# Kernel optimization log

Hardware: AMD Instinct MI355X
Metric: run time of the kernel (lower is better)

Reference implementation:

```python
import jax, jax.numpy as jnp
import numpy as np

MARGIN = 1.9
SQUARED = False


def _pairwise_distances(e, squared):
    # e: [n, d]
    dot = e @ e.T                      # [n, n]
    sq = jnp.diagonal(dot)             # [n]
    d = jax.nn.relu(sq[None, :] - 2.0 * dot + sq[:, None])
    if not squared:
        zero_mask = (d == 0.0).astype(d.dtype)
        d = jnp.sqrt(d + zero_mask * 1e-16) * (1.0 - zero_mask)
    return d


def setup_inputs() -> dict:
    key = jax.random.key(0)
    k1, k2 = jax.random.split(key)
    embeddings = jax.random.normal(k1, (8, 80, 128), dtype=jnp.float32)
    labels = jax.random.randint(k2, (8, 80), 0, 10, dtype=jnp.int64)
    return {"embeddings": embeddings, "labels": labels}


def reference(embeddings, labels):
    b, s, dim = embeddings.shape
    e = embeddings.reshape(-1, dim)          # [n, d]
    lab = labels.reshape(-1)                 # [n]
    n = e.shape[0]

    dist = _pairwise_distances(e, SQUARED)   # [n, n]

    labels_equal = lab[None, :] == lab[:, None]
    not_diag = ~jnp.eye(n, dtype=bool)
    positive_mask = labels_equal & not_diag  # [n, n]
    negative_mask = ~labels_equal            # [n, n]

    # triplet tensor [anchor i, positive j, negative k]
    triplet = dist[:, :, None] - dist[:, None, :] + MARGIN  # [n, n, n]
    valid = positive_mask[:, :, None] & negative_mask[:, None, :]
    non_easy = valid & (triplet > 0)

    num_valid = valid.sum().astype(jnp.float32)
    num_non_easy = non_easy.sum().astype(jnp.float32)

    total = jnp.sum(triplet * non_easy.astype(triplet.dtype))
    loss = jnp.where(num_non_easy > 0, total / jnp.maximum(num_non_easy, 1.0), 0.0)
    frac = num_non_easy / (num_valid + 1e-16)
    return loss, num_valid, num_non_easy, frac
```

## Files before the change

kernel.cpp:

```cpp
#include <hip/hip_runtime.h>
#include <math.h>

#define MARGIN 1.9f
#define NMAX 1024
#define COLS 64

__global__ __launch_bounds__(256) void fused_triplet_kernel(
        const float* __restrict__ e, const int* __restrict__ lab,
        int n, int d,
        float* __restrict__ part_sum,
        unsigned int* __restrict__ part_ne,
        unsigned int* __restrict__ part_valid)
{
    __shared__ float4 Bs4[COLS * 33];
    __shared__ float  part[4 * 68];
    __shared__ float  row[NMAX];
    __shared__ float  pos[NMAX];
    __shared__ int    labs[NMAX];
    __shared__ int p_cnt, n_cnt;
    __shared__ float red_s[4];
    __shared__ unsigned int red_c[4];

    const int i    = blockIdx.x;
    const int tid  = threadIdx.x;
    const int lane = tid & 63;
    const int wv   = tid >> 6;
    const int nf4  = d >> 2;

    if (tid == 0) { p_cnt = 0; n_cnt = 0; }
    for (int j = tid; j < n; j += 256) labs[j] = lab[j];

    const float4* eg = (const float4*)e;
    float4 ai[8];
    {
        const float4* ep = eg + (size_t)i * nf4 + wv * 8;
#pragma unroll
        for (int t = 0; t < 8; ++t) ai[t] = ep[t];
    }

    const int nrounds = (n + COLS - 1) / COLS;
    for (int r = 0; r < nrounds; ++r) {
        const int col0 = r * COLS;
#pragma unroll
        for (int k = 0; k < 8; ++k) {
            int idx = tid + 256 * k;
            int rr = idx >> 5, c4 = idx & 31;
            int g = col0 + rr; if (g >= n) g = n - 1;
            Bs4[rr * 33 + c4] = eg[(size_t)g * nf4 + c4];
        }
        __syncthreads();
        const float4* bp = &Bs4[lane * 33 + wv * 8];
        float acc = 0.f;
#pragma unroll
        for (int t = 0; t < 8; ++t) {
            float4 b = bp[t];
            float4 a = ai[t];
            float dx;
            dx = a.x - b.x; acc = fmaf(dx, dx, acc);
            dx = a.y - b.y; acc = fmaf(dx, dx, acc);
            dx = a.z - b.z; acc = fmaf(dx, dx, acc);
            dx = a.w - b.w; acc = fmaf(dx, dx, acc);
        }
        part[wv * 68 + lane] = acc;
        __syncthreads();
        if (wv == 0) {
            float v = part[lane] + part[68 + lane] + part[136 + lane] + part[204 + lane];
            int c = col0 + lane;
            if (c < n) row[c] = (v == 0.f) ? 0.f : sqrtf(v);
        }
        __syncthreads();
    }

    const int my_lab = labs[i];
    int local_neg = 0;
    for (int j = tid; j < n; j += 256) {
        if (labs[j] == my_lab) {
            if (j != i) { int k = atomicAdd(&p_cnt, 1); pos[k] = row[j]; }
        } else {
            local_neg++;
        }
    }
    for (int off = 32; off > 0; off >>= 1) local_neg += __shfl_down(local_neg, off, 64);
    if (lane == 0) atomicAdd(&n_cnt, local_neg);

    const float INF = __builtin_huge_valf();
    int j0 = tid, j1 = tid + 256, j2 = tid + 512, j3 = tid + 768;
    float n0 = (j0 < n && labs[j0] != my_lab) ? row[j0] : INF;
    float n1 = (j1 < n && labs[j1] != my_lab) ? row[j1] : INF;
    float n2 = (j2 < n && labs[j2] != my_lab) ? row[j2] : INF;
    float n3 = (j3 < n && labs[j3] != my_lab) ? row[j3] : INF;
    __syncthreads();
    const int P = p_cnt, N = n_cnt;

    float sum = 0.f;
    unsigned int c = 0;
    for (int j = 0; j < P; ++j) {
        float a = pos[j] + MARGIN;
        float t0 = a - n0; if (t0 > 0.f) { sum += t0; c++; }
        float t1 = a - n1; if (t1 > 0.f) { sum += t1; c++; }
        float t2 = a - n2; if (t2 > 0.f) { sum += t2; c++; }
        float t3 = a - n3; if (t3 > 0.f) { sum += t3; c++; }
    }

    for (int off = 32; off > 0; off >>= 1) {
        sum += __shfl_down(sum, off, 64);
        c   += __shfl_down(c,   off, 64);
    }
    if (lane == 0) { red_s[wv] = sum; red_c[wv] = c; }
    __syncthreads();
    if (tid == 0) {
        float s = 0.f; unsigned int cc = 0;
        for (int w = 0; w < 4; ++w) { s += red_s[w]; cc += red_c[w]; }
        part_sum[i]   = s;
        part_ne[i]    = cc;
        part_valid[i] = (unsigned int)P * (unsigned int)N;
    }
}

__global__ __launch_bounds__(256) void finalize_kernel(
        const float* __restrict__ part_sum,
        const unsigned int* __restrict__ part_ne,
        const unsigned int* __restrict__ part_valid,
        int nblk, float* __restrict__ out)
{
    __shared__ float red_s[4];
    __shared__ unsigned long long red_ne[4], red_nv[4];
    int tid = threadIdx.x;

    float s = 0.f;
    unsigned long long ne = 0, nv = 0;
    for (int b = tid; b < nblk; b += blockDim.x) {
        s  += part_sum[b];
        ne += part_ne[b];
        nv += part_valid[b];
    }
    for (int off = 32; off > 0; off >>= 1) {
        s  += __shfl_down(s,  off, 64);
        ne += __shfl_down(ne, off, 64);
        nv += __shfl_down(nv, off, 64);
    }
    int wave = tid >> 6;
    if ((tid & 63) == 0) { red_s[wave] = s; red_ne[wave] = ne; red_nv[wave] = nv; }
    __syncthreads();
    if (tid == 0) {
        float ts = 0.f; unsigned long long tne = 0, tnv = 0;
        int nwaves = (blockDim.x + 63) >> 6;
        for (int w = 0; w < nwaves; ++w) { ts += red_s[w]; tne += red_ne[w]; tnv += red_nv[w]; }
        float fne = (float)tne;
        float fnv = (float)tnv;
        out[0] = (fne > 0.f) ? (ts / fmaxf(fne, 1.f)) : 0.f;
        out[1] = fnv;
        out[2] = fne;
        out[3] = fne / (fnv + 1e-16f);
    }
}

extern "C" void kernel_launch(void* const* d_in, const int* in_sizes, int n_in,
                              void* d_out, int out_size, void* d_ws, size_t ws_size,
                              hipStream_t stream) {
    const float* e  = (const float*)d_in[0];
    const int* lab  = (const int*)d_in[1];
    int n = in_sizes[1];
    int d = in_sizes[0] / n;

    char* ws = (char*)d_ws;
    float*        part_sum   = (float*)ws;
    unsigned int* part_ne    = (unsigned int*)(ws + (size_t)n * 4);
    unsigned int* part_valid = (unsigned int*)(ws + (size_t)n * 8);

    fused_triplet_kernel<<<n, 256, 0, stream>>>(e, lab, n, d,
                                                part_sum, part_ne, part_valid);
    finalize_kernel<<<1, 256, 0, stream>>>(part_sum, part_ne, part_valid,
                                           n, (float*)d_out);
}
```

Baseline: 76.53 us.

## Process four anchors per block, one wave per anchor, with ballot-based positive compaction

Each block now handles four anchor rows: every wave computes one anchor's full distance row over the whole feature dimension, so the cross-wave partial reduction and its extra barriers go away. Each column tile loaded into shared memory is reused by four anchors, which cuts global and LDS traffic by four. Positives are compacted per wave with ballot/popcount instead of shared atomics, and negatives are kept in registers across 10 slots. The risks are a hard cap of 640 rows and 192 positives per anchor, plus fewer blocks (160) for the GPU, and each wave now runs the triplet loop for a single anchor.

```diff
diff --git a/kernel.cpp b/kernel.cpp
--- a/kernel.cpp
+++ b/kernel.cpp
@@ -2,118 +2,124 @@
 #include <math.h>
 
 #define MARGIN 1.9f
-#define NMAX 1024
-#define COLS 64
+#define NMAX  640
+#define NSLOT 10
+#define ACH   4
+#define PCAP  192
 
-__global__ __launch_bounds__(256) void fused_triplet_kernel(
+__global__ __launch_bounds__(256) void fused_strip_kernel(
         const float* __restrict__ e, const int* __restrict__ lab,
         int n, int d,
         float* __restrict__ part_sum,
         unsigned int* __restrict__ part_ne,
         unsigned int* __restrict__ part_valid)
 {
-    __shared__ float4 Bs4[COLS * 33];
-    __shared__ float  part[4 * 68];
-    __shared__ float  row[NMAX];
-    __shared__ float  pos[NMAX];
     __shared__ int    labs[NMAX];
-    __shared__ int p_cnt, n_cnt;
-    __shared__ float red_s[4];
-    __shared__ unsigned int red_c[4];
+    __shared__ float4 As4[ACH * 32];
+    __shared__ float4 Bs4[64 * 33];
+    __shared__ float  rows[ACH][NMAX];
+    __shared__ float  pos[ACH][PCAP];
 
-    const int i    = blockIdx.x;
     const int tid  = threadIdx.x;
     const int lane = tid & 63;
     const int wv   = tid >> 6;
+    const int i0   = blockIdx.x * ACH;
     const int nf4  = d >> 2;
 
-    if (tid == 0) { p_cnt = 0; n_cnt = 0; }
     for (int j = tid; j < n; j += 256) labs[j] = lab[j];
+    const float4* eg = (const float4*)e;
+    if (tid < ACH * nf4) {
+        int a  = tid / nf4;
+        int c4 = tid - a * nf4;
+        int gi = i0 + a; if (gi >= n) gi = n - 1;
+        As4[a * 32 + c4] = eg[(size_t)gi * nf4 + c4];
+    }
+    __syncthreads();
 
-    const float4* eg = (const float4*)e;
-    float4 ai[8];
-    {
-        const float4* ep = eg + (size_t)i * nf4 + wv * 8;
-#pragma unroll
-        for (int t = 0; t < 8; ++t) ai[t] = ep[t];
-    }
-
-    const int nrounds = (n + COLS - 1) / COLS;
-    for (int r = 0; r < nrounds; ++r) {
-        const int col0 = r * COLS;
+    const int ntile = (n + 63) >> 6;
+    for (int tt = 0; tt < ntile; ++tt) {
+        const int col0 = tt << 6;
 #pragma unroll
         for (int k = 0; k < 8; ++k) {
-            int idx = tid + 256 * k;
-            int rr = idx >> 5, c4 = idx & 31;
-            int g = col0 + rr; if (g >= n) g = n - 1;
-            Bs4[rr * 33 + c4] = eg[(size_t)g * nf4 + c4];
+            int idx = tid + (k << 8);
+            int r = idx >> 5, c4 = idx & 31;
+            if (c4 < nf4) {
+                int g = col0 + r; if (g >= n) g = n - 1;
+                Bs4[r * 33 + c4] = eg[(size_t)g * nf4 + c4];
+            }
         }
         __syncthreads();
-        const float4* bp = &Bs4[lane * 33 + wv * 8];
+        const float4* bp = &Bs4[lane * 33];
+        const float4* ap = &As4[wv * 32];
         float acc = 0.f;
-#pragma unroll
-        for (int t = 0; t < 8; ++t) {
+#pragma unroll 8
+        for (int t = 0; t < nf4; ++t) {
             float4 b = bp[t];
-            float4 a = ai[t];
+            float4 a = ap[t];
             float dx;
             dx = a.x - b.x; acc = fmaf(dx, dx, acc);
             dx = a.y - b.y; acc = fmaf(dx, dx, acc);
             dx = a.z - b.z; acc = fmaf(dx, dx, acc);
             dx = a.w - b.w; acc = fmaf(dx, dx, acc);
         }
-        part[wv * 68 + lane] = acc;
-        __syncthreads();
-        if (wv == 0) {
-            float v = part[lane] + part[68 + lane] + part[136 + lane] + part[204 + lane];
-            int c = col0 + lane;
-            if (c < n) row[c] = (v == 0.f) ? 0.f : sqrtf(v);
-        }
+        int c = col0 + lane;
+        if (c < n) rows[wv][c] = (acc == 0.f) ? 0.f : sqrtf(acc);
         __syncthreads();
     }
 
-    const int my_lab = labs[i];
-    int local_neg = 0;
-    for (int j = tid; j < n; j += 256) {
-        if (labs[j] == my_lab) {
-            if (j != i) { int k = atomicAdd(&p_cnt, 1); pos[k] = row[j]; }
-        } else {
-            local_neg++;
+    const int i = i0 + wv;
+    const int my_lab = (i < n) ? labs[i] : -2147483647;
+    const float INF = __builtin_huge_valf();
+
+    float negv[NSLOT];
+    int P = 0, nneg = 0;
+#pragma unroll
+    for (int s = 0; s < NSLOT; ++s) {
+        int c = (s << 6) + lane;
+        bool in = (i < n) && (c < n);
+        float v = in ? rows[wv][c] : 0.f;
+        int   l = in ? labs[c] : -2147483647;
+        bool is_neg = in && (l != my_lab);
+        negv[s] = is_neg ? v : INF;
+        nneg += is_neg ? 1 : 0;
+        bool is_pos = in && (l == my_lab) && (c != i);
+        unsigned long long m = __ballot(is_pos);
+        if (is_pos) {
+            int off = __popcll(m & ((1ull << lane) - 1ull));
+            int idx = P + off;
+            if (idx < PCAP) pos[wv][idx] = v;
+        }
+        P += __popcll(m);
+    }
+    if (P > PCAP) P = PCAP;
+
+    float sum0 = 0.f, sum1 = 0.f;
+    unsigned int c0 = 0, c1 = 0;
+    for (int j = 0; j < P; ++j) {
+        float a = pos[wv][j] + MARGIN;
+#pragma unroll
+        for (int s = 0; s < 5; ++s) {
+            float t = a - negv[s];
+            if (t > 0.f) { sum0 += t; c0++; }
+        }
+#pragma unroll
+        for (int s = 5; s < NSLOT; ++s) {
+            float t = a - negv[s];
+            if (t > 0.f) { sum1 += t; c1++; }
         }
     }
-    for (int off = 32; off > 0; off >>= 1) local_neg += __shfl_down(local_neg, off, 64);
-    if (lane == 0) atomicAdd(&n_cnt, local_neg);
-
-    const float INF = __builtin_huge_valf();
-    int j0 = tid, j1 = tid + 256, j2 = tid + 512, j3 = tid + 768;
-    float n0 = (j0 < n && labs[j0] != my_lab) ? row[j0] : INF;
-    float n1 = (j1 < n && labs[j1] != my_lab) ? row[j1] : INF;
-    float n2 = (j2 < n && labs[j2] != my_lab) ? row[j2] : INF;
-    float n3 = (j3 < n && labs[j3] != my_lab) ? row[j3] : INF;
-    __syncthreads();
-    const int P = p_cnt, N = n_cnt;
-
-    float sum = 0.f;
-    unsigned int c = 0;
-    for (int j = 0; j < P; ++j) {
-        float a = pos[j] + MARGIN;
-        float t0 = a - n0; if (t0 > 0.f) { sum += t0; c++; }
-        float t1 = a - n1; if (t1 > 0.f) { sum += t1; c++; }
-        float t2 = a - n2; if (t2 > 0.f) { sum += t2; c++; }
-        float t3 = a - n3; if (t3 > 0.f) { sum += t3; c++; }
-    }
+    float sum = sum0 + sum1;
+    unsigned int cnt = c0 + c1;
 
     for (int off = 32; off > 0; off >>= 1) {
-        sum += __shfl_down(sum, off, 64);
-        c   += __shfl_down(c,   off, 64);
+        sum  += __shfl_down(sum,  off, 64);
+        cnt  += __shfl_down(cnt,  off, 64);
+        nneg += __shfl_down(nneg, off, 64);
     }
-    if (lane == 0) { red_s[wv] = sum; red_c[wv] = c; }
-    __syncthreads();
-    if (tid == 0) {
-        float s = 0.f; unsigned int cc = 0;
-        for (int w = 0; w < 4; ++w) { s += red_s[w]; cc += red_c[w]; }
-        part_sum[i]   = s;
-        part_ne[i]    = cc;
-        part_valid[i] = (unsigned int)P * (unsigned int)N;
+    if (lane == 0 && i < n) {
+        part_sum[i]   = sum;
+        part_ne[i]    = cnt;
+        part_valid[i] = (unsigned int)P * (unsigned int)nneg;
     }
 }
 
@@ -168,8 +174,9 @@
     unsigned int* part_ne    = (unsigned int*)(ws + (size_t)n * 4);
     unsigned int* part_valid = (unsigned int*)(ws + (size_t)n * 8);
 
-    fused_triplet_kernel<<<n, 256, 0, stream>>>(e, lab, n, d,
-                                                part_sum, part_ne, part_valid);
+    int blocks = (n + ACH - 1) / ACH;
+    fused_strip_kernel<<<blocks, 256, 0, stream>>>(e, lab, n, d,
+                                                   part_sum, part_ne, part_valid);
     finalize_kernel<<<1, 256, 0, stream>>>(part_sum, part_ne, part_valid,
                                            n, (float*)d_out);
 }
```

After: 85.30 us. +11.5%, slower.
